# Kernel tuning notes

Hardware: AMD Instinct MI355X
Metric: run time of the kernel (lower is better)

The kernel has to match this reference:

```python
import jax, jax.numpy as jnp
import numpy as np

EMBED_DIM = 1024
N_HEADS = 16
HEAD_DIM = EMBED_DIM // N_HEADS


def setup_inputs() -> dict:
    key = jax.random.key(0)
    ks = jax.random.split(key, 8)
    B, Tq, Tk, C = 2, 2048, 2048, EMBED_DIM
    s = 1.0 / np.sqrt(C)
    return {
        "query": jax.random.normal(ks[0], (B, Tq, C), jnp.float32),
        "context": jax.random.normal(ks[1], (B, Tk, C), jnp.float32),
        "Wq": jax.random.normal(ks[2], (C, C), jnp.float32) * s,
        "bq": jnp.zeros((C,), jnp.float32),
        "Wkv": jax.random.normal(ks[3], (C, 2 * C), jnp.float32) * s,
        "bkv": jnp.zeros((2 * C,), jnp.float32),
        "Wo": jax.random.normal(ks[4], (C, C), jnp.float32) * s,
        "bo": jnp.zeros((C,), jnp.float32),
    }


def reference(query, context, Wq, bq, Wkv, bkv, Wo, bo):
    B, Tq, C = query.shape
    Tk = context.shape[1]
    H, D = N_HEADS, HEAD_DIM
    # projections
    q = (query @ Wq + bq).reshape(B, Tq, H, D)        # [B,Tq,H,D]
    kv = (context @ Wkv + bkv).reshape(B, Tk, 2, H, D)
    k = kv[:, :, 0]                                   # [B,Tk,H,D]
    v = kv[:, :, 1]
    scale = D ** -0.5
    # attention scores [B,H,Tq,Tk]
    attn = jnp.einsum("bqhd,bkhd->bhqk", q, k) * scale
    attn = jax.nn.softmax(attn, axis=-1)
    # dropout p=0.0 -> identity in eval / p=0
    out = jnp.einsum("bhqk,bkhd->bqhd", attn, v).reshape(B, Tq, C)
    return out @ Wo + bo
```

## Files before the change

kernel.cpp:

```cpp
#include <hip/hip_runtime.h>
#include <math.h>

typedef unsigned short u16;
typedef unsigned int u32;
typedef __attribute__((ext_vector_type(8))) short short8;
typedef __attribute__((ext_vector_type(4))) short short4v;
typedef __attribute__((ext_vector_type(4))) float f32x4;

__device__ __forceinline__ u16 f2bf(float f) {
  union { float f; unsigned u; } x; x.f = f;
  unsigned r = x.u + 0x7FFFu + ((x.u >> 16) & 1u);
  return (u16)(r >> 16);
}

__device__ __forceinline__ u32 asu(float f) {
  union { float f; u32 u; } x; x.f = f; return x.u;
}

__device__ __forceinline__ u32 pack2bf(float a, float b) {
  return __builtin_amdgcn_perm(asu(b) + 0x8000u, asu(a) + 0x8000u, 0x07060302u);
}

__device__ __forceinline__ u32 cvtpk2bf(float a, float b) {
  u32 r;
  asm("v_cvt_pk_bf16_f32 %0, %1, %2" : "=v"(r) : "v"(a), "v"(b));
  return r;
}

__device__ __forceinline__ void gld_lds16(const void* g, void* l) {
  __builtin_amdgcn_global_load_lds(
      (const __attribute__((address_space(1))) unsigned int*)g,
      (__attribute__((address_space(3))) unsigned int*)l, 16, 0, 0);
}

__global__ void pre_kernel(const float* __restrict__ q, const float* __restrict__ c,
                           const float* __restrict__ Wq, const float* __restrict__ Wkv,
                           const float* __restrict__ Wo,
                           u16* __restrict__ xq, u16* __restrict__ xc,
                           u16* __restrict__ WqF, u16* __restrict__ WkvF,
                           u16* __restrict__ WoF) {
  __shared__ float tile[32][33];
  int bx = blockIdx.x;
  int t = threadIdx.y * 32 + threadIdx.x;
  if (bx < 8192) {
    int i = bx * 256 + t;
    const float* src = q; u16* dst = xq;
    if (i >= 1048576) { i -= 1048576; src = c; dst = xc; }
    float4 v = ((const float4*)src)[i];
    ((uint2*)dst)[i] = make_uint2(
        (unsigned)f2bf(v.x) | ((unsigned)f2bf(v.y) << 16),
        (unsigned)f2bf(v.z) | ((unsigned)f2bf(v.w) << 16));
  } else {
    int g = bx - 8192;
    int gx = g & 127, gy = g >> 7;
    const float* src; u16* dst; int N, n0;
    if (gx < 32)      { src = Wq;  dst = WqF;  N = 1024; n0 = gx * 32; }
    else if (gx < 96) { src = Wkv; dst = WkvF; N = 2048; n0 = (gx - 32) * 32; }
    else              { src = Wo;  dst = WoF;  N = 1024; n0 = (gx - 96) * 32; }
    int k0 = gy * 32;
    int tx = threadIdx.x, ty = threadIdx.y;
#pragma unroll
    for (int i = 0; i < 4; ++i)
      tile[ty * 4 + i][tx] = src[(size_t)(k0 + ty * 4 + i) * N + n0 + tx];
    __syncthreads();
    int e = t * 4;
    int ch = e >> 9, rem = e & 511;
    int kg = (rem >> 7) & 3;
    int nl = (rem >> 3) & 15;
    int j0 = rem & 7;
    int kk = kg * 8 + j0;
    int nn = ch * 16 + nl;
    u32 lo = pack2bf(tile[kk][nn], tile[kk + 1][nn]);
    u32 hi = pack2bf(tile[kk + 2][nn], tile[kk + 3][nn]);
    *(uint2*)(dst + (size_t)(((n0 >> 4) + ch) * 32 + gy) * 512 + rem) = make_uint2(lo, hi);
  }
}

__global__ __launch_bounds__(256) void qkv_gemm(
    const u16* __restrict__ Xq, const u16* __restrict__ Xc,
    const u16* __restrict__ WqF, const u16* __restrict__ WkvF,
    const float* __restrict__ bq, const float* __restrict__ bkv,
    u16* __restrict__ qb, u16* __restrict__ kf, u16* __restrict__ vf,
    float qscale) {
  __shared__ __align__(16) u16 smem[16896];
  const int tid = threadIdx.x, lane = tid & 63, wave = tid >> 6;
  const int quad = lane >> 4, cl = lane & 15;
  const int wr = (wave >> 1) * 64, wc = (wave & 1) * 64;

  int x = blockIdx.x;
  const u16 *A, *Bf; const float* bias; int m0, n0; bool isq;
  if (x < 256) {
    isq = true;  A = Xq; Bf = WqF;  bias = bq;
    m0 = (x >> 3) * 128; n0 = (x & 7) * 128;
  } else {
    isq = false; x -= 256; A = Xc; Bf = WkvF; bias = bkv;
    m0 = (x >> 4) * 128; n0 = (x & 15) * 128;
  }
  const int bn4 = (n0 + wc) >> 4;

  const int rA = lane >> 3;
  const int kcs = ((lane & 7) ^ rA) * 8;
  const int r7 = cl & 7;

  auto stageA = [&](int k0, int buf) {
    u16* As = smem + buf * 8192;
#pragma unroll
    for (int it = 0; it < 4; ++it) {
      int chunk = it * 4 + wave;
      gld_lds16(A + (size_t)(m0 + chunk * 8 + rA) * 1024 + k0 + kcs, As + chunk * 512);
    }
  };

  f32x4 acc[4][4] = {};

  stageA(0, 0);
  __syncthreads();

  for (int i = 0; i < 16; ++i) {
    const int k0 = i * 64;
    const int cur = i & 1;
    if (i < 15) stageA(k0 + 64, cur ^ 1);
    const u16* As = smem + cur * 8192;
    short8 bf[2][4];
#pragma unroll
    for (int ks = 0; ks < 2; ++ks)
#pragma unroll
      for (int ni = 0; ni < 4; ++ni)
        bf[ks][ni] = *(const short8*)(Bf + (size_t)((bn4 + ni) * 32 + (k0 >> 5) + ks) * 512 + lane * 8);
#pragma unroll
    for (int ks = 0; ks < 2; ++ks) {
      short8 af[4];
#pragma unroll
      for (int mi = 0; mi < 4; ++mi) {
        int row = wr + mi * 16 + cl;
        af[mi] = *(const short8*)(As + (row >> 3) * 512 + r7 * 64 +
                                  (((ks << 2) | quad) ^ r7) * 8);
      }
#pragma unroll
      for (int mi = 0; mi < 4; ++mi)
#pragma unroll
        for (int ni = 0; ni < 4; ++ni)
          acc[mi][ni] = __builtin_amdgcn_mfma_f32_16x16x32_bf16(af[mi], bf[ks][ni], acc[mi][ni], 0, 0, 0);
    }
    __syncthreads();
  }

  if (isq) {
#pragma unroll
    for (int mi = 0; mi < 4; ++mi)
#pragma unroll
      for (int ni = 0; ni < 4; ++ni)
#pragma unroll
        for (int r = 0; r < 4; ++r) {
          int row = m0 + wr + mi * 16 + quad * 4 + r;
          int col = n0 + wc + ni * 16 + cl;
          qb[(size_t)row * 1024 + col] = f2bf((acc[mi][ni][r] + bias[col]) * qscale);
        }
    return;
  }

  const int b = m0 >> 11, kt0 = (m0 & 2047) >> 6;
  const bool kreg = (n0 < 1024);
  if (kreg) {
#pragma unroll
    for (int mi = 0; mi < 4; ++mi)
#pragma unroll
      for (int ni = 0; ni < 4; ++ni)
#pragma unroll
        for (int r = 0; r < 4; ++r)
          smem[(wr + mi * 16 + quad * 4 + r) * 132 + wc + ni * 16 + cl] =
              f2bf(acc[mi][ni][r] + bias[n0 + wc + ni * 16 + cl]);
    __syncthreads();
#pragma unroll
    for (int i = 0; i < 8; ++i) {
      int c = i * 4 + wave;
      int hs = c >> 4, ts = (c >> 3) & 1, ks = (c >> 2) & 1, idx = c & 3;
      int h = (n0 >> 6) + hs;
      size_t bhkt = ((size_t)((b * 16 + h) * 32 + kt0 + ts)) * 4096;
      short8 v = *(const short8*)(smem + (ts * 64 + idx * 16 + cl) * 132 +
                                  hs * 64 + ks * 32 + quad * 8);
      *(short8*)(kf + bhkt + (size_t)(ks * 4 + idx) * 512 + lane * 8) = v;
    }
  } else {
#pragma unroll
    for (int mi = 0; mi < 4; ++mi)
#pragma unroll
      for (int ni = 0; ni < 4; ++ni) {
        float v0 = acc[mi][ni][0] + bias[n0 + wc + ni * 16 + cl];
        float v1 = acc[mi][ni][1] + bias[n0 + wc + ni * 16 + cl];
        float v2 = acc[mi][ni][2] + bias[n0 + wc + ni * 16 + cl];
        float v3 = acc[mi][ni][3] + bias[n0 + wc + ni * 16 + cl];
        *(uint2*)(smem + (wc + ni * 16 + cl) * 132 + wr + mi * 16 + quad * 4) =
            make_uint2(pack2bf(v0, v1), pack2bf(v2, v3));
      }
    __syncthreads();
#pragma unroll
    for (int i = 0; i < 8; ++i) {
      int c = i * 4 + wave;
      int hs = c >> 4, ts = (c >> 3) & 1, ks = (c >> 2) & 1, idx = c & 3;
      int h = ((n0 - 1024) >> 6) + hs;
      size_t bhkt = ((size_t)((b * 16 + h) * 32 + kt0 + ts)) * 4096;
      const u16* src = smem + (hs * 64 + idx * 16 + cl) * 132 + ts * 64 + ks * 32 + quad * 4;
      short8 v;
      *(short4v*)&v       = *(const short4v*)(src);
      *((short4v*)&v + 1) = *(const short4v*)(src + 16);
      *(short8*)(vf + bhkt + (size_t)(ks * 4 + idx) * 512 + lane * 8) = v;
    }
  }
}

__global__ __launch_bounds__(256) void o_gemm(
    const u16* __restrict__ A, const u16* __restrict__ Bf,
    const float* __restrict__ bias, float* __restrict__ Cm) {
  __shared__ __align__(16) u16 As[2][64 * 64];
  const int tid = threadIdx.x, lane = tid & 63, wave = tid >> 6;
  const int quad = lane >> 4, cl = lane & 15;
  const int m0 = (blockIdx.x >> 3) * 64, n0 = (blockIdx.x & 7) * 128;
  const int wr = (wave >> 1) * 32, wc = (wave & 1) * 64;
  const int bn4 = (n0 + wc) >> 4;

  const int rA = lane >> 3;
  const int kcs = ((lane & 7) ^ rA) * 8;
  const int r7 = cl & 7;

  auto stageA = [&](int k0, int buf) {
#pragma unroll
    for (int it = 0; it < 2; ++it) {
      int chunk = wave * 2 + it;
      gld_lds16(A + (size_t)(m0 + chunk * 8 + rA) * 1024 + k0 + kcs, As[buf] + chunk * 512);
    }
  };

  f32x4 acc[2][4] = {};

  stageA(0, 0);
  __syncthreads();

  for (int i = 0; i < 16; ++i) {
    const int k0 = i * 64;
    const int cur = i & 1;
    if (i < 15) stageA(k0 + 64, cur ^ 1);
    short8 bf[2][4];
#pragma unroll
    for (int ks = 0; ks < 2; ++ks)
#pragma unroll
      for (int ni = 0; ni < 4; ++ni)
        bf[ks][ni] = *(const short8*)(Bf + (size_t)((bn4 + ni) * 32 + (k0 >> 5) + ks) * 512 + lane * 8);
#pragma unroll
    for (int ks = 0; ks < 2; ++ks) {
      short8 af[2];
#pragma unroll
      for (int mi = 0; mi < 2; ++mi) {
        int row = wr + mi * 16 + cl;
        af[mi] = *(const short8*)(As[cur] + (row >> 3) * 512 + r7 * 64 +
                                  (((ks << 2) | quad) ^ r7) * 8);
      }
#pragma unroll
      for (int mi = 0; mi < 2; ++mi)
#pragma unroll
        for (int ni = 0; ni < 4; ++ni)
          acc[mi][ni] = __builtin_amdgcn_mfma_f32_16x16x32_bf16(af[mi], bf[ks][ni], acc[mi][ni], 0, 0, 0);
    }
    __syncthreads();
  }
#pragma unroll
  for (int mi = 0; mi < 2; ++mi)
#pragma unroll
    for (int ni = 0; ni < 4; ++ni)
#pragma unroll
      for (int r = 0; r < 4; ++r) {
        int row = m0 + wr + mi * 16 + quad * 4 + r;
        int col = n0 + wc + ni * 16 + cl;
        Cm[(size_t)row * 1024 + col] = acc[mi][ni][r] + bias[col];
      }
}

__global__ __launch_bounds__(256, 4) void flash_attn(
    const u16* __restrict__ qb, const u16* __restrict__ kf,
    const u16* __restrict__ vf, u16* __restrict__ outp) {
  __shared__ __align__(16) u16 kv[2][16 * 512];
  const int tid = threadIdx.x, lane = tid & 63, wave = tid >> 6;
  const int quad = lane >> 4, cl = lane & 15;
  const int id = blockIdx.x;
  const int h = (id & 7) | (((id >> 3) & 1) << 3);
  const int b = (id >> 4) & 1;
  const int qt = id >> 5;

  const int qrow0 = b * 2048 + qt * 64 + wave * 16;
  short8 bq[2];
#pragma unroll
  for (int ks = 0; ks < 2; ++ks)
    bq[ks] = *(const short8*)(qb + (size_t)(qrow0 + cl) * 1024 + h * 64 + ks * 32 + quad * 8);

  short8 ones;
#pragma unroll
  for (int j = 0; j < 8; ++j) ones[j] = (short)0x3F80;

  const u16* kfb = kf + (size_t)((b * 16 + h) * 32) * 4096;
  const u16* vfb = vf + (size_t)((b * 16 + h) * 32) * 4096;

  auto stage = [&](int kt, int buf) {
#pragma unroll
    for (int i = 0; i < 2; ++i) {
      int c = wave * 2 + i;
      gld_lds16(kfb + (size_t)kt * 4096 + c * 512 + lane * 8, &kv[buf][c * 512]);
      gld_lds16(vfb + (size_t)kt * 4096 + c * 512 + lane * 8, &kv[buf][(8 + c) * 512]);
    }
  };

  f32x4 o_acc[4] = {};
  f32x4 l_acc = {};

  stage(0, 0);
  __syncthreads();

#pragma unroll 1
  for (int kt = 0; kt < 32; ++kt) {
    const int cur = kt & 1, nxt = cur ^ 1;
    if (kt < 31) stage(kt + 1, nxt);
    const u16* kb = &kv[cur][0];
    const u16* vb = &kv[cur][8 * 512];
    f32x4 st[4] = {};
    __builtin_amdgcn_s_setprio(1);
#pragma unroll
    for (int ks = 0; ks < 2; ++ks)
#pragma unroll
      for (int ni = 0; ni < 4; ++ni) {
        short8 ak = *(const short8*)(kb + (ks * 4 + ni) * 512 + lane * 8);
        st[ni] = __builtin_amdgcn_mfma_f32_16x16x32_bf16(ak, bq[ks], st[ni], 0, 0, 0);
      }
    __builtin_amdgcn_s_setprio(0);
    short8 av[2][4];
#pragma unroll
    for (int ks = 0; ks < 2; ++ks)
#pragma unroll
      for (int nd = 0; nd < 4; ++nd)
        av[ks][nd] = *(const short8*)(vb + (ks * 4 + nd) * 512 + lane * 8);
    u32 bp[2][4];
#pragma unroll
    for (int ni = 0; ni < 4; ++ni) {
      float p0 = __builtin_amdgcn_exp2f(st[ni][0]);
      float p1 = __builtin_amdgcn_exp2f(st[ni][1]);
      float p2 = __builtin_amdgcn_exp2f(st[ni][2]);
      float p3 = __builtin_amdgcn_exp2f(st[ni][3]);
      bp[ni >> 1][(ni & 1) * 2 + 0] = cvtpk2bf(p0, p1);
      bp[ni >> 1][(ni & 1) * 2 + 1] = cvtpk2bf(p2, p3);
    }
    __builtin_amdgcn_s_setprio(1);
#pragma unroll
    for (int ks = 0; ks < 2; ++ks) {
      short8 pb;
      *(u32*)&pb     = bp[ks][0];
      ((u32*)&pb)[1] = bp[ks][1];
      ((u32*)&pb)[2] = bp[ks][2];
      ((u32*)&pb)[3] = bp[ks][3];
#pragma unroll
      for (int nd = 0; nd < 4; ++nd)
        o_acc[nd] = __builtin_amdgcn_mfma_f32_16x16x32_bf16(av[ks][nd], pb, o_acc[nd], 0, 0, 0);
      l_acc = __builtin_amdgcn_mfma_f32_16x16x32_bf16(ones, pb, l_acc, 0, 0, 0);
    }
    __builtin_amdgcn_s_setprio(0);
    __syncthreads();
  }
  float inv = 1.f / l_acc[0];
  u16* Ow = &kv[0][wave * 16 * 68];
#pragma unroll
  for (int nd = 0; nd < 4; ++nd)
#pragma unroll
    for (int r2 = 0; r2 < 2; ++r2)
      *(u32*)(Ow + cl * 68 + nd * 16 + quad * 4 + r2 * 2) =
          cvtpk2bf(o_acc[nd][r2 * 2] * inv, o_acc[nd][r2 * 2 + 1] * inv);
#pragma unroll
  for (int half = 0; half < 2; ++half) {
    int row = half * 8 + (lane >> 3);
    int d0 = (lane & 7) * 8;
    short8 ov = *(const short8*)(Ow + row * 68 + d0);
    *(short8*)(outp + (size_t)(qrow0 + row) * 1024 + h * 64 + d0) = ov;
  }
}

extern "C" void kernel_launch(void* const* d_in, const int* in_sizes, int n_in,
                              void* d_out, int out_size, void* d_ws, size_t ws_size,
                              hipStream_t stream) {
  const float* query   = (const float*)d_in[0];
  const float* context = (const float*)d_in[1];
  const float* Wq  = (const float*)d_in[2];
  const float* bq  = (const float*)d_in[3];
  const float* Wkv = (const float*)d_in[4];
  const float* bkv = (const float*)d_in[5];
  const float* Wo  = (const float*)d_in[6];
  const float* bo  = (const float*)d_in[7];
  float* out = (float*)d_out;

  char* ws = (char*)d_ws;
  size_t off = 0;
  auto alloc = [&](size_t bytes) {
    char* p = ws + off;
    off += (bytes + 255) & ~(size_t)255;
    return p;
  };
  u16* buf0 = (u16*)alloc(4096ull * 1024 * 2);
  u16* xcb  = (u16*)alloc(4096ull * 1024 * 2);
  u16* WqF  = (u16*)alloc(1024ull * 1024 * 2);
  u16* WkvF = (u16*)alloc(2048ull * 1024 * 2);
  u16* WoF  = (u16*)alloc(1024ull * 1024 * 2);
  u16* qb   = (u16*)alloc(4096ull * 1024 * 2);
  u16* kfr  = (u16*)alloc(4ull * 1024 * 1024 * 2);
  u16* vfr  = (u16*)alloc(4ull * 1024 * 1024 * 2);

  const float QSCALE = 0.125f * 1.44269504f;

  pre_kernel<<<12288, dim3(32, 8), 0, stream>>>(query, context, Wq, Wkv, Wo,
                                                buf0, xcb, WqF, WkvF, WoF);
  qkv_gemm<<<768, 256, 0, stream>>>(buf0, xcb, WqF, WkvF, bq, bkv,
                                    qb, kfr, vfr, QSCALE);
  flash_attn<<<1024, 256, 0, stream>>>(qb, kfr, vfr, buf0);
  o_gemm<<<512, 256, 0, stream>>>(buf0, WoF, bo, out);
}
```

Baseline: 198.9 us.

## Stage B tiles through LDS and remap GEMM blocks for XCD locality

In both the QKV and output-projection GEMMs, B-operand fragments are now loaded asynchronously into double-buffered shared memory alongside the A tiles, instead of being read straight from global memory inside the compute loop. Block indices are also remapped so that blocks sharing the same XCD work on neighbouring M/N tiles, with the KV work scheduled before the Q work. The goal is to hide global-load latency for B and improve L2 reuse per XCD. In exchange the kernels use more LDS per block, which can lower occupancy.

Result: faster. 186.0 us (-6.5%).

```diff
diff --git a/kernel.cpp b/kernel.cpp
--- a/kernel.cpp
+++ b/kernel.cpp
@@ -82,21 +82,24 @@
     const float* __restrict__ bq, const float* __restrict__ bkv,
     u16* __restrict__ qb, u16* __restrict__ kf, u16* __restrict__ vf,
     float qscale) {
-  __shared__ __align__(16) u16 smem[16896];
+  __shared__ __align__(16) u16 smem[32768];
   const int tid = threadIdx.x, lane = tid & 63, wave = tid >> 6;
   const int quad = lane >> 4, cl = lane & 15;
   const int wr = (wave >> 1) * 64, wc = (wave & 1) * 64;
 
-  int x = blockIdx.x;
+  const int xcd = blockIdx.x & 7, pos = blockIdx.x >> 3;
   const u16 *A, *Bf; const float* bias; int m0, n0; bool isq;
-  if (x < 256) {
+  if (pos < 64) {
+    isq = false; A = Xc; Bf = WkvF; bias = bkv;
+    m0 = ((xcd >> 1) * 8 + (pos >> 3)) * 128;
+    n0 = ((xcd & 1) * 8 + (pos & 7)) * 128;
+  } else {
+    int p = pos - 64;
     isq = true;  A = Xq; Bf = WqF;  bias = bq;
-    m0 = (x >> 3) * 128; n0 = (x & 7) * 128;
-  } else {
-    isq = false; x -= 256; A = Xc; Bf = WkvF; bias = bkv;
-    m0 = (x >> 4) * 128; n0 = (x & 15) * 128;
-  }
-  const int bn4 = (n0 + wc) >> 4;
+    m0 = (xcd * 4 + (p >> 3)) * 128;
+    n0 = (p & 7) * 128;
+  }
+  const int n04 = n0 >> 4;
 
   const int rA = lane >> 3;
   const int kcs = ((lane & 7) ^ rA) * 8;
@@ -110,23 +113,35 @@
       gld_lds16(A + (size_t)(m0 + chunk * 8 + rA) * 1024 + k0 + kcs, As + chunk * 512);
     }
   };
+  auto stageB = [&](int k0, int buf) {
+    u16* Bs = smem + 16384 + buf * 8192;
+    const int k05 = k0 >> 5;
+#pragma unroll
+    for (int it = 0; it < 4; ++it) {
+      int c = it * 4 + wave;
+      int j = c >> 1, ks = c & 1;
+      gld_lds16(Bf + (size_t)((n04 + j) * 32 + k05 + ks) * 512 + lane * 8, Bs + c * 512);
+    }
+  };
 
   f32x4 acc[4][4] = {};
 
   stageA(0, 0);
+  stageB(0, 0);
   __syncthreads();
 
   for (int i = 0; i < 16; ++i) {
     const int k0 = i * 64;
     const int cur = i & 1;
-    if (i < 15) stageA(k0 + 64, cur ^ 1);
+    if (i < 15) { stageA(k0 + 64, cur ^ 1); stageB(k0 + 64, cur ^ 1); }
     const u16* As = smem + cur * 8192;
+    const u16* Bs = smem + 16384 + cur * 8192;
     short8 bf[2][4];
 #pragma unroll
     for (int ks = 0; ks < 2; ++ks)
 #pragma unroll
       for (int ni = 0; ni < 4; ++ni)
-        bf[ks][ni] = *(const short8*)(Bf + (size_t)((bn4 + ni) * 32 + (k0 >> 5) + ks) * 512 + lane * 8);
+        bf[ks][ni] = *(const short8*)(Bs + (size_t)((((wave & 1) * 4 + ni) * 2 + ks) * 512) + lane * 8);
 #pragma unroll
     for (int ks = 0; ks < 2; ++ks) {
       short8 af[4];
@@ -212,47 +227,62 @@
 __global__ __launch_bounds__(256) void o_gemm(
     const u16* __restrict__ A, const u16* __restrict__ Bf,
     const float* __restrict__ bias, float* __restrict__ Cm) {
-  __shared__ __align__(16) u16 As[2][64 * 64];
+  __shared__ __align__(16) u16 smem[24576];
   const int tid = threadIdx.x, lane = tid & 63, wave = tid >> 6;
   const int quad = lane >> 4, cl = lane & 15;
-  const int m0 = (blockIdx.x >> 3) * 64, n0 = (blockIdx.x & 7) * 128;
+  const int xcd = blockIdx.x & 7, pos = blockIdx.x >> 3;
+  const int m0 = (xcd * 8 + (pos >> 3)) * 64, n0 = (pos & 7) * 128;
   const int wr = (wave >> 1) * 32, wc = (wave & 1) * 64;
-  const int bn4 = (n0 + wc) >> 4;
+  const int n04 = n0 >> 4;
 
   const int rA = lane >> 3;
   const int kcs = ((lane & 7) ^ rA) * 8;
   const int r7 = cl & 7;
 
   auto stageA = [&](int k0, int buf) {
+    u16* As = smem + buf * 4096;
 #pragma unroll
     for (int it = 0; it < 2; ++it) {
       int chunk = wave * 2 + it;
-      gld_lds16(A + (size_t)(m0 + chunk * 8 + rA) * 1024 + k0 + kcs, As[buf] + chunk * 512);
+      gld_lds16(A + (size_t)(m0 + chunk * 8 + rA) * 1024 + k0 + kcs, As + chunk * 512);
+    }
+  };
+  auto stageB = [&](int k0, int buf) {
+    u16* Bs = smem + 8192 + buf * 8192;
+    const int k05 = k0 >> 5;
+#pragma unroll
+    for (int it = 0; it < 4; ++it) {
+      int c = it * 4 + wave;
+      int j = c >> 1, ks = c & 1;
+      gld_lds16(Bf + (size_t)((n04 + j) * 32 + k05 + ks) * 512 + lane * 8, Bs + c * 512);
     }
   };
 
   f32x4 acc[2][4] = {};
 
   stageA(0, 0);
+  stageB(0, 0);
   __syncthreads();
 
   for (int i = 0; i < 16; ++i) {
     const int k0 = i * 64;
     const int cur = i & 1;
-    if (i < 15) stageA(k0 + 64, cur ^ 1);
+    if (i < 15) { stageA(k0 + 64, cur ^ 1); stageB(k0 + 64, cur ^ 1); }
+    const u16* As = smem + cur * 4096;
+    const u16* Bs = smem + 8192 + cur * 8192;
     short8 bf[2][4];
 #pragma unroll
     for (int ks = 0; ks < 2; ++ks)
 #pragma unroll
       for (int ni = 0; ni < 4; ++ni)
-        bf[ks][ni] = *(const short8*)(Bf + (size_t)((bn4 + ni) * 32 + (k0 >> 5) + ks) * 512 + lane * 8);
+        bf[ks][ni] = *(const short8*)(Bs + (size_t)((((wave & 1) * 4 + ni) * 2 + ks) * 512) + lane * 8);
 #pragma unroll
     for (int ks = 0; ks < 2; ++ks) {
       short8 af[2];
 #pragma unroll
       for (int mi = 0; mi < 2; ++mi) {
         int row = wr + mi * 16 + cl;
-        af[mi] = *(const short8*)(As[cur] + (row >> 3) * 512 + r7 * 64 +
+        af[mi] = *(const short8*)(As + (row >> 3) * 512 + r7 * 64 +
                                   (((ks << 2) | quad) ^ r7) * 8);
       }
 #pragma unroll
```
